# Optimization experiments

Measured on AMD Instinct MI355X. Metric: run time of the kernel, lower is better.

Reference implementation:

```python
import jax, jax.numpy as jnp
import numpy as np

M, D, NI, L, NPL, R, T = 2, 128, 131072, 4, 2048, 8, 32
N = NI + L * NPL  # total DAG nodes


def setup_inputs() -> dict:
    key = jax.random.key(0)
    ks = jax.random.split(key, 18)
    thax = jax.random.randint(ks[0], (NI,), 0, T)
    sine = jax.random.uniform(ks[1], (NI,), jnp.float32)
    # parents of layer-l deriv nodes index any node built earlier (topological)
    raw = jax.random.randint(ks[2], (L, NPL, 2), 0, 2**30)
    bounds = jnp.array([NI + l * NPL for l in range(L)])[:, None, None]
    par = raw % bounds
    ridx = jax.random.randint(ks[3], (L, NPL), 0, R)
    pos = jax.random.uniform(ks[4], (N,), jnp.float32) + 0.01
    neg = jax.random.uniform(ks[5], (N,), jnp.float32) + 0.01
    s = 0.05
    return {
        'thax': thax, 'sine': sine, 'par': par, 'ridx': ridx,
        'pos': pos, 'neg': neg,
        'init_table': jax.random.normal(ks[6], (M, T, D)) * s,
        's_vec': jax.random.normal(ks[7], (M, D)) * s,
        'W1': jax.random.normal(ks[8], (M, R, 2 * D, D)) * s,
        'b1': jax.random.normal(ks[9], (M, R, D)) * s,
        'W2': jax.random.normal(ks[10], (M, R, D, D)) * s,
        'b2': jax.random.normal(ks[11], (M, R, D)) * s,
        'tweaks': jax.random.normal(ks[12], (M, 1, 2)) * s,
        'We1': jax.random.normal(ks[13], (M, D, D)) * s,
        'be1': jax.random.normal(ks[14], (M, D)) * s,
        'we2': jax.random.normal(ks[15], (M, D)) * s,
        'be2': jax.random.normal(ks[16], (M,)) * s,
    }


def reference(thax, sine, par, ridx, pos, neg, init_table, s_vec,
              W1, b1, W2, b2, tweaks, We1, be1, we2, be2):
    # init nodes: thax embedding + sine embellishment (per model)
    emb0 = init_table[:, thax, :] + sine[None, :, None] * s_vec[:, None, :]  # [M,NI,D]
    store = jnp.zeros((M, N, D), emb0.dtype).at[:, :NI].set(emb0)
    # topological layers of deriv nodes: gather parents, rule-indexed 2-layer MLP
    for l in range(L):
        p, r = par[l], ridx[l]
        cat = store[:, p].reshape(M, NPL, 2 * D)               # gather parents
        h = jax.nn.relu(jnp.einsum('mnc,mncd->mnd', cat, W1[:, r]) + b1[:, r])
        out = (jnp.einsum('mnd,mnde->mne', h, W2[:, r]) + b2[:, r]
               + tweaks[:, 0, 1][:, None, None])
        store = store.at[:, NI + l * NPL: NI + (l + 1) * NPL].set(out)
    # eval_net: per-node scalar logit (+ per-problem tweak)
    he = jax.nn.relu(jnp.einsum('mnd,mde->mne', store, We1) + be1[:, None, :])
    logit = jnp.einsum('mnd,md->mn', he, we2) + be2[:, None] + tweaks[:, 0, 0][:, None]
    tot_pos, tot_neg = pos.sum(), neg.sum()
    pw = tot_neg / tot_pos  # POS_WEIGHT_EXTRA = 1.0
    gold = pos / (pos + neg)
    w = pos + neg
    # BCEWithLogitsLoss(pos_weight=pw) per node, weighted by (pos+neg)
    bce = -(pw * gold[None] * jax.nn.log_sigmoid(logit)
            + (1.0 - gold[None]) * jax.nn.log_sigmoid(-logit))
    loss = (w[None] * bce).sum(axis=1)                          # [M]
    posOK = jnp.where(logit >= 0, pos[None], 0.0).sum(axis=1)
    negOK = jnp.where(logit < 0, neg[None], 0.0).sum(axis=1)
    return (loss, posOK, negOK, tot_pos, tot_neg)
```

## Files before the change

### kernel.cpp

```cpp
#include <hip/hip_runtime.h>
#include <hip/hip_bf16.h>

#define M_ 2
#define D_ 128
#define NI_ 131072
#define L_ 4
#define NPL_ 2048
#define R_ 8
#define T_ 32
#define N_ (NI_ + L_ * NPL_)
#define ND_ (L_ * NPL_)
#define PART3_ 1344

typedef __bf16 bf16x8 __attribute__((ext_vector_type(8)));
typedef float f32x4 __attribute__((ext_vector_type(4)));

#define OFF_W1T    0u
#define OFF_W2T    1048576u
#define OFF_WE1T   1572864u
#define OFF_TAB    1638400u
#define OFF_SVEC   1654784u
#define OFF_SORTED 1655296u
#define OFF_STARTS 1688064u
#define OFF_CNTF   1688192u
#define OFF_CNTA   1688320u
#define OFF_EA2    1688448u
#define OFF_EWB    1721216u
#define OFF_PA     1723264u
#define OFF_PB     1734016u
#define OFF_PPOK   1744768u
#define OFF_PNOK   1755520u
#define OFF_PTP    1766272u
#define OFF_PTN    1771648u
#define OFF_G      1777024u
#define OFF_STORE  2317696u
#define OFF_FSG    6512000u
#define OFF_CFG    6512032u
#define OFF_FLIST  6512064u

__device__ __forceinline__ unsigned short f2bu(float f) {
  unsigned int u = __float_as_uint(f);
  u += 0x7fffu + ((u >> 16) & 1u);
  return (unsigned short)(u >> 16);
}
__device__ __forceinline__ bf16x8 ldb8(const unsigned short* p) {
  return *reinterpret_cast<const bf16x8*>(p);
}

__device__ __forceinline__ bf16x8 node_chunk(int m, int row, int d0,
    const unsigned short* tab, const unsigned short* svec,
    const unsigned short* sd, const int* thax, const float* sine) {
  if (row < NI_) {
    bf16x8 tv = ldb8(&tab[(m * T_ + thax[row]) * D_ + d0]);
    bf16x8 sv = ldb8(&svec[m * D_ + d0]);
    float sn = sine[row];
    bf16x8 r;
#pragma unroll
    for (int j = 0; j < 8; ++j)
      r[j] = (__bf16)((float)tv[j] + sn * (float)sv[j]);
    return r;
  }
  return ldb8(&sd[(size_t)(m * ND_ + (row - NI_)) * D_ + d0]);
}

__global__ __launch_bounds__(256) void megaprep_kernel(
    const float* W1, const float* W2, const float* We1,
    const float* init_table, const float* s_vec,
    const float* b1, const float* be1, const float* we2,
    const int* ridx, const int* par,
    unsigned short* W1T, unsigned short* W2T, unsigned short* We1T,
    unsigned short* tab, unsigned short* svec,
    float* G, float* EA2, float* EWB,
    int* sorted, int* starts, int* cntF, int* cntA,
    int* fsg, int* cfg, int* fastlist, unsigned int* pzero) {
  __shared__ float smem[1056];
  __shared__ int icnt[16], ioff[16];
  int job = blockIdx.x;
  int tid = threadIdx.x;

  if (job < 800) {
    int z, rblk, cblk;
    if (job < 512)      { z = job >> 5;            rblk = (job & 31) >> 2; cblk = job & 3; }
    else if (job < 768) { int q = job - 512; z = 16 + (q >> 4); rblk = (q & 15) >> 2; cblk = q & 3; }
    else                { int q = job - 768; z = 32 + (q >> 4); rblk = (q & 15) >> 2; cblk = q & 3; }
    const float* src; unsigned short* dst; int R;
    if (z < 16)      { src = W1  + (size_t)z * 32768;        dst = W1T  + (size_t)z * 32768;        R = 256; }
    else if (z < 32) { src = W2  + (size_t)(z - 16) * 16384; dst = W2T  + (size_t)(z - 16) * 16384; R = 128; }
    else             { src = We1 + (size_t)(z - 32) * 16384; dst = We1T + (size_t)(z - 32) * 16384; R = 128; }
    int r0 = rblk * 32, c0 = cblk * 32;
    float (*tile)[33] = (float(*)[33])smem;
    int tx = tid & 31, ty = tid >> 5;
#pragma unroll
    for (int k = 0; k < 4; ++k)
      tile[ty + 8 * k][tx] = src[(size_t)(r0 + ty + 8 * k) * D_ + c0 + tx];
    __syncthreads();
#pragma unroll
    for (int k = 0; k < 4; ++k)
      dst[(size_t)(c0 + ty + 8 * k) * R + r0 + tx] = f2bu(tile[tx][ty + 8 * k]);
  } else if (job == 800) {
    for (int i = tid; i < 8448; i += 256) {
      if (i < 8192) tab[i] = f2bu(init_table[i]);
      else svec[i - 8192] = f2bu(s_vec[i - 8192]);
    }
  } else if (job < 1329) {
    int q = job - 801;
    int t = q / 16, mr = q & 15;
    int m = mr >> 3;
    int slot = tid >> 7, e = tid & 127;
    const float* vec = (t < 32) ? &init_table[(size_t)(m * T_ + t) * D_]
                                : &s_vec[(size_t)m * D_];
    if (tid < 128) smem[tid] = vec[tid];
    __syncthreads();
    const float* w = &W1[((size_t)mr * 256 + slot * 128) * D_];
    float acc = 0.f;
#pragma unroll 8
    for (int c = 0; c < 128; ++c) acc = fmaf(smem[c], w[c * D_ + e], acc);
    if (slot == 0 && t < 32) acc += b1[mr * D_ + e];
    G[((size_t)(mr * 2 + slot) * 33 + t) * D_ + e] = acc;
  } else if (job < 1363) {
    int q = job - 1329;
    int m = q / 17, t = (q % 17) * 2 + (tid >> 7);
    int e = tid & 127;
    if (t <= 32) {
      const float* vec = (t < 32) ? &init_table[(size_t)(m * T_ + t) * D_]
                                  : &s_vec[(size_t)m * D_];
      const float* w = &We1[(size_t)m * D_ * D_];
      float acc = 0.f;
#pragma unroll 8
      for (int d = 0; d < 128; ++d) acc = fmaf(vec[d], w[d * D_ + e], acc);
      if (t < 32) {
        EA2[m * 4096 + ((e >> 1) * 32 + t) * 2 + (e & 1)] = acc + be1[m * D_ + e];
      } else {
        EWB[(m * D_ + e) * 2 + 0] = acc;
        EWB[(m * D_ + e) * 2 + 1] = we2[m * D_ + e];
      }
    }
  } else if (job < 1367) {
    int l = job - 1363;
    if (tid < 16) icnt[tid] = 0;
    __syncthreads();
    for (int n = tid; n < NPL_; n += 256) {
      int r = ridx[l * NPL_ + n];
      int p0 = par[(l * NPL_ + n) * 2 + 0], p1 = par[(l * NPL_ + n) * 2 + 1];
      int slow = (p0 >= NI_ || p1 >= NI_) ? 1 : 0;
      atomicAdd(&icnt[r * 2 + slow], 1);
    }
    __syncthreads();
    if (tid == 0) {
      int run = 0;
      for (int b = 0; b < 16; ++b) { ioff[b] = run; run += icnt[b]; }
      for (int r = 0; r < R_; ++r) {
        starts[l * R_ + r] = ioff[2 * r];
        cntF[l * R_ + r] = icnt[2 * r];
        cntA[l * R_ + r] = icnt[2 * r] + icnt[2 * r + 1];
      }
    }
    __syncthreads();
    for (int n = tid; n < NPL_; n += 256) {
      int r = ridx[l * NPL_ + n];
      int p0 = par[(l * NPL_ + n) * 2 + 0], p1 = par[(l * NPL_ + n) * 2 + 1];
      int slow = (p0 >= NI_ || p1 >= NI_) ? 1 : 0;
      int p = atomicAdd(&ioff[r * 2 + slow], 1);
      sorted[l * NPL_ + p] = n;
    }
  } else if (job == 1367) {
    if (tid < 8) icnt[tid] = 0;
    __syncthreads();
    for (int g = tid; g < ND_; g += 256) {
      int p0 = par[2 * g], p1 = par[2 * g + 1];
      if (p0 < NI_ && p1 < NI_) atomicAdd(&icnt[ridx[g]], 1);
    }
    __syncthreads();
    if (tid == 0) {
      int run = 0;
      for (int r = 0; r < R_; ++r) {
        ioff[r] = run; fsg[r] = run; cfg[r] = icnt[r]; run += icnt[r];
      }
    }
    __syncthreads();
    for (int g = tid; g < ND_; g += 256) {
      int p0 = par[2 * g], p1 = par[2 * g + 1];
      if (p0 < NI_ && p1 < NI_) {
        int p = atomicAdd(&ioff[ridx[g]], 1);
        fastlist[p] = g;
      }
    }
  } else {
    for (int i = tid; i < 13440; i += 256) pzero[i] = 0u;
  }
}

__global__ __launch_bounds__(256) void main_kernel(
    const int* thax, const float* sine, const int* par,
    const float* pos, const float* neg,
    const float* b2, const float* tweaks,
    const float* G, const unsigned short* W2T, const unsigned short* We1T,
    const float* EA2, const float* EWB,
    const float* be1, const float* we2, const float* be2,
    const int* fsg, const int* cfg, const int* fastlist,
    unsigned short* sd,
    float* pA, float* pB, float* pPok, float* pNok, float* pTp, float* pTn) {
  __shared__ float sbuf[4448];
  int bid = blockIdx.x;
  int tid = threadIdx.x;
  int w = tid >> 6, lane = tid & 63;

  if (bid < 1280) {
    int m = bid / 640, q = bid % 640;
    int r = q / 80, tile = q % 80;
    int cnt = cfg[r];
    int base = tile * 16;
    if (base >= cnt) return;
    unsigned short* h_lds = (unsigned short*)sbuf;
    int*   t0a  = (int*)(sbuf + 1024);
    int*   t1a  = t0a + 16;
    float* s0a  = (float*)(t1a + 16);
    float* s1a  = s0a + 16;
    int*   gida = (int*)(s1a + 16);
    float* red2 = sbuf + 1104;
    if (tid < 16) {
      int loc = base + tid; if (loc >= cnt) loc = cnt - 1;
      int gid = fastlist[fsg[r] + loc];
      int p0 = par[2 * gid], p1 = par[2 * gid + 1];
      t0a[tid] = thax[p0]; s0a[tid] = sine[p0];
      t1a[tid] = thax[p1]; s1a[tid] = sine[p1];
      gida[tid] = gid;
    }
    __syncthreads();
    const float* Gm = &G[(size_t)(m * R_ + r) * 8448];
    {
      int row = tid >> 4, seg = tid & 15, d0 = seg * 8;
      int t0 = t0a[row], t1 = t1a[row];
      float s0 = s0a[row], s1 = s1a[row];
      const float* pa = &Gm[t0 * 128 + d0];
      const float* pb = &Gm[(33 + t1) * 128 + d0];
      const float* pu = &Gm[4096 + d0];
      const float* pv = &Gm[8320 + d0];
      bf16x8 hv;
#pragma unroll
      for (int half = 0; half < 2; ++half) {
        float4 a = *(const float4*)(pa + half * 4);
        float4 b = *(const float4*)(pb + half * 4);
        float4 u = *(const float4*)(pu + half * 4);
        float4 v = *(const float4*)(pv + half * 4);
        hv[half * 4 + 0] = (__bf16)fmaxf(a.x + b.x + s0 * u.x + s1 * v.x, 0.f);
        hv[half * 4 + 1] = (__bf16)fmaxf(a.y + b.y + s0 * u.y + s1 * v.y, 0.f);
        hv[half * 4 + 2] = (__bf16)fmaxf(a.z + b.z + s0 * u.z + s1 * v.z, 0.f);
        hv[half * 4 + 3] = (__bf16)fmaxf(a.w + b.w + s0 * u.w + s1 * v.w, 0.f);
      }
      *(bf16x8*)&h_lds[row * 128 + (d0 ^ ((row & 7) << 3))] = hv;
    }
    __syncthreads();
    int l15 = lane & 15, l4 = lane >> 4;
    const unsigned short* w2b = &W2T[(size_t)(m * R_ + r) * D_ * D_];
    f32x4 acc[2];
    acc[0] = (f32x4){0.f, 0.f, 0.f, 0.f};
    acc[1] = (f32x4){0.f, 0.f, 0.f, 0.f};
#pragma unroll
    for (int kc = 0; kc < 4; ++kc) {
      int d0 = kc * 32 + l4 * 8;
      bf16x8 a2 = ldb8(&h_lds[l15 * 128 + (d0 ^ ((l15 & 7) << 3))]);
#pragma unroll
      for (int f = 0; f < 2; ++f) {
        int fg = w * 2 + f;
        bf16x8 b = ldb8(&w2b[(fg * 16 + l15) * D_ + d0]);
        acc[f] = __builtin_amdgcn_mfma_f32_16x16x32_bf16(a2, b, acc[f], 0, 0, 0);
      }
    }
    float tw1 = tweaks[m * 2 + 1];
    const float* b2v = &b2[(m * R_ + r) * D_];
    __syncthreads();
#pragma unroll
    for (int i = 0; i < 4; ++i) {
      int row = l4 * 4 + i;
      int g = base + row;
#pragma unroll
      for (int f = 0; f < 2; ++f) {
        int e = (w * 2 + f) * 16 + l15;
        unsigned short val = f2bu(acc[f][i] + b2v[e] + tw1);
        h_lds[row * 128 + (e ^ ((row & 7) << 3))] = val;
        if (g < cnt) sd[(size_t)(m * ND_ + gida[row]) * D_ + e] = val;
      }
    }
    __syncthreads();
    f32x4 ae[2];
    ae[0] = (f32x4){0.f, 0.f, 0.f, 0.f};
    ae[1] = (f32x4){0.f, 0.f, 0.f, 0.f};
    const unsigned short* we1b = &We1T[(size_t)m * D_ * D_];
#pragma unroll
    for (int kc = 0; kc < 4; ++kc) {
      int d0 = kc * 32 + l4 * 8;
      bf16x8 a2 = ldb8(&h_lds[l15 * 128 + (d0 ^ ((l15 & 7) << 3))]);
#pragma unroll
      for (int f = 0; f < 2; ++f) {
        int fg = w * 2 + f;
        bf16x8 b = ldb8(&we1b[(fg * 16 + l15) * D_ + d0]);
        ae[f] = __builtin_amdgcn_mfma_f32_16x16x32_bf16(a2, b, ae[f], 0, 0, 0);
      }
    }
    float part[4] = {0.f, 0.f, 0.f, 0.f};
#pragma unroll
    for (int f = 0; f < 2; ++f) {
      int e = (w * 2 + f) * 16 + l15;
      float bb = be1[m * D_ + e];
      float wv = we2[m * D_ + e];
#pragma unroll
      for (int i = 0; i < 4; ++i) {
        float he = ae[f][i] + bb;
        he = he > 0.f ? he : 0.f;
        part[i] += he * wv;
      }
    }
#pragma unroll
    for (int mask = 1; mask < 16; mask <<= 1) {
#pragma unroll
      for (int i = 0; i < 4; ++i) part[i] += __shfl_xor(part[i], mask, 64);
    }
    if (l15 == 0) {
#pragma unroll
      for (int i = 0; i < 4; ++i) red2[w * 16 + l4 * 4 + i] = part[i];
    }
    __syncthreads();
    if (tid < 16) {
      int g = base + tid;
      float v6[6] = {0.f, 0.f, 0.f, 0.f, 0.f, 0.f};
      if (g < cnt) {
        float logit = red2[tid] + red2[16 + tid] + red2[32 + tid] + red2[48 + tid]
                    + be2[m] + tweaks[m * 2 + 0];
        int grow = NI_ + gida[tid];
        float p_ = pos[grow], n_ = neg[grow];
        float lse = log1pf(__expf(-fabsf(logit)));
        v6[0] = p_ * (fmaxf(-logit, 0.f) + lse);
        v6[1] = n_ * (fmaxf(logit, 0.f) + lse);
        v6[2] = logit >= 0.f ? p_ : 0.f;
        v6[3] = logit < 0.f ? n_ : 0.f;
        v6[4] = p_; v6[5] = n_;
      }
#pragma unroll
      for (int mask = 1; mask < 16; mask <<= 1) {
#pragma unroll
        for (int qq = 0; qq < 6; ++qq) v6[qq] += __shfl_xor(v6[qq], mask, 64);
      }
      if (tid == 0) {
        int slot = 512 + r * 80 + tile;
        pA[m * PART3_ + slot] = v6[0];
        pB[m * PART3_ + slot] = v6[1];
        pPok[m * PART3_ + slot] = v6[2];
        pNok[m * PART3_ + slot] = v6[3];
        if (m == 0) { pTp[slot] = v6[4]; pTn[slot] = v6[5]; }
      }
    }
  } else {
    int q = bid - 1280;
    int m = q >> 9, xb = q & 511;
    float* lea = sbuf;
    float* lwb = sbuf + 4096;
    float* red = sbuf + 4352;
    for (int i = tid; i < 4096; i += 256) lea[i] = EA2[m * 4096 + i];
    if (tid < 256) lwb[tid] = EWB[m * 256 + tid];
    __syncthreads();
    int row = xb * 256 + tid;
    int t = thax[row];
    float s = sine[row];
    float acc = 0.f;
#pragma unroll 8
    for (int p = 0; p < 64; ++p) {
      float2 ea = *(const float2*)&lea[(p * 32 + t) * 2];
      float4 wb = *(const float4*)&lwb[p * 4];
      float x0 = fmaf(s, wb.x, ea.x); x0 = fmaxf(x0, 0.f);
      acc = fmaf(x0, wb.y, acc);
      float x1 = fmaf(s, wb.z, ea.y); x1 = fmaxf(x1, 0.f);
      acc = fmaf(x1, wb.w, acc);
    }
    float logit = acc + be2[m] + tweaks[m * 2 + 0];
    float p_ = pos[row], n_ = neg[row];
    float lse = log1pf(__expf(-fabsf(logit)));
    float v[6];
    v[0] = p_ * (fmaxf(-logit, 0.f) + lse);
    v[1] = n_ * (fmaxf(logit, 0.f) + lse);
    v[2] = logit >= 0.f ? p_ : 0.f;
    v[3] = logit < 0.f ? n_ : 0.f;
    v[4] = p_; v[5] = n_;
#pragma unroll
    for (int mask = 1; mask < 64; mask <<= 1) {
#pragma unroll
      for (int k = 0; k < 6; ++k) v[k] += __shfl_xor(v[k], mask, 64);
    }
    if (lane == 0) {
#pragma unroll
      for (int k = 0; k < 6; ++k) red[k * 16 + w] = v[k];
    }
    __syncthreads();
    if (tid == 0) {
      float t6[6];
#pragma unroll
      for (int k = 0; k < 6; ++k)
        t6[k] = red[k * 16 + 0] + red[k * 16 + 1] + red[k * 16 + 2] + red[k * 16 + 3];
      pA[m * PART3_ + xb] = t6[0];
      pB[m * PART3_ + xb] = t6[1];
      pPok[m * PART3_ + xb] = t6[2];
      pNok[m * PART3_ + xb] = t6[3];
      if (m == 0) { pTp[xb] = t6[4]; pTn[xb] = t6[5]; }
    }
  }
}

__global__ __launch_bounds__(128) void slow_eval_kernel(int l,
    const int* thax, const float* sine, const int* par,
    const float* b1, const float* b2, const float* tweaks,
    const float* pos, const float* neg,
    const float* be1, const float* we2, const float* be2,
    const unsigned short* tab, const unsigned short* svec,
    const unsigned short* W1T, const unsigned short* W2T,
    const unsigned short* We1T,
    const int* sorted, const int* starts, const int* cntF, const int* cntA,
    unsigned short* sd,
    float* pA, float* pB, float* pPok, float* pNok, float* pTp, float* pTn) {
  int tile = blockIdx.x, r = blockIdx.y, m = blockIdx.z;
  int cF = cntF[l * R_ + r];
  int cS = cntA[l * R_ + r] - cF;
  int base = tile * 16;
  if (base >= cS) return;
  int start = starts[l * R_ + r] + cF;
  int tid = threadIdx.x;
  int w = tid >> 6, lane = tid & 63;
  int l15 = lane & 15, l4 = lane >> 4;
  __shared__ unsigned short h_lds[16 * 128];
  __shared__ float red2[32];

  int loc = base + l15; if (loc >= cS) loc = cS - 1;
  int node = sorted[l * NPL_ + start + loc];
  int p0 = par[(l * NPL_ + node) * 2 + 0];
  int p1 = par[(l * NPL_ + node) * 2 + 1];
  const unsigned short* w1b = &W1T[(size_t)(m * R_ + r) * D_ * 256];
  const unsigned short* w2b = &W2T[(size_t)(m * R_ + r) * D_ * D_];
  const unsigned short* we1b = &We1T[(size_t)m * D_ * D_];

  bf16x8 av[8];
#pragma unroll
  for (int kc = 0; kc < 8; ++kc) {
    int k = kc * 32 + l4 * 8;
    int p = (k < 128) ? p0 : p1;
    av[kc] = node_chunk(m, p, k & 127, tab, svec, sd, thax, sine);
  }
  f32x4 acch[4];
#pragma unroll
  for (int f = 0; f < 4; ++f) acch[f] = (f32x4){0.f, 0.f, 0.f, 0.f};
#pragma unroll
  for (int kc = 0; kc < 8; ++kc) {
    int k = kc * 32 + l4 * 8;
#pragma unroll
    for (int f = 0; f < 4; ++f) {
      int fg = w * 4 + f;
      bf16x8 b = ldb8(&w1b[(fg * 16 + l15) * 256 + k]);
      acch[f] = __builtin_amdgcn_mfma_f32_16x16x32_bf16(av[kc], b, acch[f], 0, 0, 0);
    }
  }
  const float* b1v = &b1[(m * R_ + r) * D_];
#pragma unroll
  for (int f = 0; f < 4; ++f) {
    int d = (w * 4 + f) * 16 + l15;
    float bb = b1v[d];
#pragma unroll
    for (int i = 0; i < 4; ++i) {
      int row = l4 * 4 + i;
      float h = acch[f][i] + bb;
      h = h > 0.f ? h : 0.f;
      h_lds[row * 128 + (d ^ ((row & 7) << 3))] = f2bu(h);
    }
  }
  __syncthreads();
  f32x4 acco[4];
#pragma unroll
  for (int f = 0; f < 4; ++f) acco[f] = (f32x4){0.f, 0.f, 0.f, 0.f};
#pragma unroll
  for (int kc = 0; kc < 4; ++kc) {
    int d0 = kc * 32 + l4 * 8;
    bf16x8 a2 = ldb8(&h_lds[l15 * 128 + (d0 ^ ((l15 & 7) << 3))]);
#pragma unroll
    for (int f = 0; f < 4; ++f) {
      int fg = w * 4 + f;
      bf16x8 b = ldb8(&w2b[(fg * 16 + l15) * D_ + d0]);
      acco[f] = __builtin_amdgcn_mfma_f32_16x16x32_bf16(a2, b, acco[f], 0, 0, 0);
    }
  }
  float tw1 = tweaks[m * 2 + 1];
  const float* b2v = &b2[(m * R_ + r) * D_];
  __syncthreads();
#pragma unroll
  for (int i = 0; i < 4; ++i) {
    int row = l4 * 4 + i;
    int g = base + row;
#pragma unroll
    for (int f = 0; f < 4; ++f) {
      int e = (w * 4 + f) * 16 + l15;
      unsigned short val = f2bu(acco[f][i] + b2v[e] + tw1);
      h_lds[row * 128 + (e ^ ((row & 7) << 3))] = val;
      if (g < cS) {
        int nd = sorted[l * NPL_ + start + g];
        sd[(size_t)(m * ND_ + l * NPL_ + nd) * D_ + e] = val;
      }
    }
  }
  __syncthreads();
  f32x4 ae[4];
#pragma unroll
  for (int f = 0; f < 4; ++f) ae[f] = (f32x4){0.f, 0.f, 0.f, 0.f};
#pragma unroll
  for (int kc = 0; kc < 4; ++kc) {
    int d0 = kc * 32 + l4 * 8;
    bf16x8 a2 = ldb8(&h_lds[l15 * 128 + (d0 ^ ((l15 & 7) << 3))]);
#pragma unroll
    for (int f = 0; f < 4; ++f) {
      int fg = w * 4 + f;
      bf16x8 b = ldb8(&we1b[(fg * 16 + l15) * D_ + d0]);
      ae[f] = __builtin_amdgcn_mfma_f32_16x16x32_bf16(a2, b, ae[f], 0, 0, 0);
    }
  }
  float part[4] = {0.f, 0.f, 0.f, 0.f};
#pragma unroll
  for (int f = 0; f < 4; ++f) {
    int e = (w * 4 + f) * 16 + l15;
    float bb = be1[m * D_ + e];
    float wv = we2[m * D_ + e];
#pragma unroll
    for (int i = 0; i < 4; ++i) {
      float he = ae[f][i] + bb;
      he = he > 0.f ? he : 0.f;
      part[i] += he * wv;
    }
  }
#pragma unroll
  for (int mask = 1; mask < 16; mask <<= 1) {
#pragma unroll
    for (int i = 0; i < 4; ++i) part[i] += __shfl_xor(part[i], mask, 64);
  }
  if (l15 == 0) {
#pragma unroll
    for (int i = 0; i < 4; ++i) red2[w * 16 + l4 * 4 + i] = part[i];
  }
  __syncthreads();
  if (tid < 16) {
    int g = base + tid;
    float v6[6] = {0.f, 0.f, 0.f, 0.f, 0.f, 0.f};
    if (g < cS) {
      float logit = red2[tid] + red2[16 + tid] + be2[m] + tweaks[m * 2 + 0];
      int nd = sorted[l * NPL_ + start + g];
      int grow = NI_ + l * NPL_ + nd;
      float p_ = pos[grow], n_ = neg[grow];
      float lse = log1pf(__expf(-fabsf(logit)));
      v6[0] = p_ * (fmaxf(-logit, 0.f) + lse);
      v6[1] = n_ * (fmaxf(logit, 0.f) + lse);
      v6[2] = logit >= 0.f ? p_ : 0.f;
      v6[3] = logit < 0.f ? n_ : 0.f;
      v6[4] = p_; v6[5] = n_;
    }
#pragma unroll
    for (int mask = 1; mask < 16; mask <<= 1) {
#pragma unroll
      for (int qq = 0; qq < 6; ++qq) v6[qq] += __shfl_xor(v6[qq], mask, 64);
    }
    if (tid == 0) {
      int slot = 1152 + (l - 1) * 64 + r * 8 + tile;
      pA[m * PART3_ + slot] = v6[0];
      pB[m * PART3_ + slot] = v6[1];
      pPok[m * PART3_ + slot] = v6[2];
      pNok[m * PART3_ + slot] = v6[3];
      if (m == 0) { pTp[slot] = v6[4]; pTn[slot] = v6[5]; }
    }
  }
}

__global__ __launch_bounds__(256) void finalize_kernel(
    const float* pA, const float* pB, const float* pPok, const float* pNok,
    const float* pTp, const float* pTn, float* out) {
  __shared__ float lred[10][4];
  const float* srcs[10] = {pA, pA + PART3_, pB, pB + PART3_,
                           pPok, pPok + PART3_, pNok, pNok + PART3_,
                           pTp, pTn};
  int tid = threadIdx.x;
  int w = tid >> 6, lane = tid & 63;
#pragma unroll
  for (int q = 0; q < 10; ++q) {
    float s = 0.f;
    for (int i = tid; i < PART3_; i += 256) s += srcs[q][i];
#pragma unroll
    for (int mask = 1; mask < 64; mask <<= 1) s += __shfl_xor(s, mask, 64);
    if (lane == 0) lred[q][w] = s;
  }
  __syncthreads();
  if (tid == 0) {
    float totals[10];
#pragma unroll
    for (int q = 0; q < 10; ++q)
      totals[q] = lred[q][0] + lred[q][1] + lred[q][2] + lred[q][3];
    float tp = totals[8], tn = totals[9];
    float pw = tn / tp;
    out[0] = pw * totals[0] + totals[2];
    out[1] = pw * totals[1] + totals[3];
    out[2] = totals[4]; out[3] = totals[5];
    out[4] = totals[6]; out[5] = totals[7];
    out[6] = tp; out[7] = tn;
  }
}

extern "C" void kernel_launch(void* const* d_in, const int* in_sizes, int n_in,
                              void* d_out, int out_size, void* d_ws, size_t ws_size,
                              hipStream_t stream) {
  const int*   thax = (const int*)d_in[0];
  const float* sine = (const float*)d_in[1];
  const int*   par  = (const int*)d_in[2];
  const int*   ridx = (const int*)d_in[3];
  const float* pos  = (const float*)d_in[4];
  const float* neg  = (const float*)d_in[5];
  const float* init_table = (const float*)d_in[6];
  const float* s_vec = (const float*)d_in[7];
  const float* W1 = (const float*)d_in[8];
  const float* b1 = (const float*)d_in[9];
  const float* W2 = (const float*)d_in[10];
  const float* b2 = (const float*)d_in[11];
  const float* tweaks = (const float*)d_in[12];
  const float* We1 = (const float*)d_in[13];
  const float* be1 = (const float*)d_in[14];
  const float* we2 = (const float*)d_in[15];
  const float* be2 = (const float*)d_in[16];

  char* ws = (char*)d_ws;
  unsigned short* W1T  = (unsigned short*)(ws + OFF_W1T);
  unsigned short* W2T  = (unsigned short*)(ws + OFF_W2T);
  unsigned short* We1T = (unsigned short*)(ws + OFF_WE1T);
  unsigned short* tab  = (unsigned short*)(ws + OFF_TAB);
  unsigned short* svec = (unsigned short*)(ws + OFF_SVEC);
  int* sorted = (int*)(ws + OFF_SORTED);
  int* starts = (int*)(ws + OFF_STARTS);
  int* cntF   = (int*)(ws + OFF_CNTF);
  int* cntA   = (int*)(ws + OFF_CNTA);
  float* EA2  = (float*)(ws + OFF_EA2);
  float* EWB  = (float*)(ws + OFF_EWB);
  float* pA   = (float*)(ws + OFF_PA);
  float* pB   = (float*)(ws + OFF_PB);
  float* pPok = (float*)(ws + OFF_PPOK);
  float* pNok = (float*)(ws + OFF_PNOK);
  float* pTp  = (float*)(ws + OFF_PTP);
  float* pTn  = (float*)(ws + OFF_PTN);
  float* G    = (float*)(ws + OFF_G);
  unsigned short* sd = (unsigned short*)(ws + OFF_STORE);
  int* fsg      = (int*)(ws + OFF_FSG);
  int* cfg      = (int*)(ws + OFF_CFG);
  int* fastlist = (int*)(ws + OFF_FLIST);

  megaprep_kernel<<<1369, 256, 0, stream>>>(
      W1, W2, We1, init_table, s_vec, b1, be1, we2, ridx, par,
      W1T, W2T, We1T, tab, svec, G, EA2, EWB, sorted, starts, cntF, cntA,
      fsg, cfg, fastlist, (unsigned int*)pA);
  main_kernel<<<2304, 256, 0, stream>>>(
      thax, sine, par, pos, neg, b2, tweaks, G, W2T, We1T, EA2, EWB,
      be1, we2, be2, fsg, cfg, fastlist, sd,
      pA, pB, pPok, pNok, pTp, pTn);
  for (int l = 1; l < L_; ++l) {
    slow_eval_kernel<<<dim3(8, R_, M_), 128, 0, stream>>>(
        l, thax, sine, par, b1, b2, tweaks, pos, neg, be1, we2, be2,
        tab, svec, W1T, W2T, We1T, sorted, starts, cntF, cntA, sd,
        pA, pB, pPok, pNok, pTp, pTn);
  }
  finalize_kernel<<<1, 256, 0, stream>>>(pA, pB, pPok, pNok, pTp, pTn,
                                         (float*)d_out);
}
```

Before: 100.7 us.

## Merge per-layer slow-eval launches and finalize into one persistent tail kernel

Replaces the three per-layer slow_eval launches and the separate finalize launch with a single tail kernel of two 512-thread blocks, one per model. Each block walks layers 1..3 sequentially, with wavefronts taking tiles round-robin and using block barriers between layers in place of kernel boundaries. Each wavefront now computes all 128 output columns itself, using wave-local LDS waits instead of block syncs. Deriv-node pos/neg totals move into two extra main_kernel blocks, which shrinks the partial arrays. The aim is to cut launch and dependency gaps, at the cost of running the serial tail on only two CUs with less parallelism per layer.

Result: slower. 364.6 us (+262.1%).

```diff
diff --git a/kernel.cpp b/kernel.cpp
--- a/kernel.cpp
+++ b/kernel.cpp
@@ -10,7 +10,7 @@
 #define T_ 32
 #define N_ (NI_ + L_ * NPL_)
 #define ND_ (L_ * NPL_)
-#define PART3_ 1344
+#define PART4_ 1184
 
 typedef __bf16 bf16x8 __attribute__((ext_vector_type(8)));
 typedef float f32x4 __attribute__((ext_vector_type(4)));
@@ -27,16 +27,16 @@
 #define OFF_EA2    1688448u
 #define OFF_EWB    1721216u
 #define OFF_PA     1723264u
-#define OFF_PB     1734016u
-#define OFF_PPOK   1744768u
-#define OFF_PNOK   1755520u
-#define OFF_PTP    1766272u
-#define OFF_PTN    1771648u
-#define OFF_G      1777024u
-#define OFF_STORE  2317696u
-#define OFF_FSG    6512000u
-#define OFF_CFG    6512032u
-#define OFF_FLIST  6512064u
+#define OFF_PB     1732736u
+#define OFF_PPOK   1742208u
+#define OFF_PNOK   1751680u
+#define OFF_PTP    1761152u
+#define OFF_PTN    1765888u
+#define OFF_G      1770624u
+#define OFF_STORE  2311296u
+#define OFF_FSG    6505600u
+#define OFF_CFG    6505632u
+#define OFF_FLIST  6505664u
 
 __device__ __forceinline__ unsigned short f2bu(float f) {
   unsigned int u = __float_as_uint(f);
@@ -186,7 +186,7 @@
       }
     }
   } else {
-    for (int i = tid; i < 13440; i += 256) pzero[i] = 0u;
+    for (int i = tid; i < 11840; i += 256) pzero[i] = 0u;
   }
 }
 
@@ -323,7 +323,7 @@
     __syncthreads();
     if (tid < 16) {
       int g = base + tid;
-      float v6[6] = {0.f, 0.f, 0.f, 0.f, 0.f, 0.f};
+      float v6[4] = {0.f, 0.f, 0.f, 0.f};
       if (g < cnt) {
         float logit = red2[tid] + red2[16 + tid] + red2[32 + tid] + red2[48 + tid]
                     + be2[m] + tweaks[m * 2 + 0];
@@ -334,23 +334,21 @@
         v6[1] = n_ * (fmaxf(logit, 0.f) + lse);
         v6[2] = logit >= 0.f ? p_ : 0.f;
         v6[3] = logit < 0.f ? n_ : 0.f;
-        v6[4] = p_; v6[5] = n_;
       }
 #pragma unroll
       for (int mask = 1; mask < 16; mask <<= 1) {
 #pragma unroll
-        for (int qq = 0; qq < 6; ++qq) v6[qq] += __shfl_xor(v6[qq], mask, 64);
+        for (int qq = 0; qq < 4; ++qq) v6[qq] += __shfl_xor(v6[qq], mask, 64);
       }
       if (tid == 0) {
         int slot = 512 + r * 80 + tile;
-        pA[m * PART3_ + slot] = v6[0];
-        pB[m * PART3_ + slot] = v6[1];
-        pPok[m * PART3_ + slot] = v6[2];
-        pNok[m * PART3_ + slot] = v6[3];
-        if (m == 0) { pTp[slot] = v6[4]; pTn[slot] = v6[5]; }
-      }
-    }
-  } else {
+        pA[m * PART4_ + slot] = v6[0];
+        pB[m * PART4_ + slot] = v6[1];
+        pPok[m * PART4_ + slot] = v6[2];
+        pNok[m * PART4_ + slot] = v6[3];
+      }
+    }
+  } else if (bid < 2304) {
     int q = bid - 1280;
     int m = q >> 9, xb = q & 511;
     float* lea = sbuf;
@@ -396,16 +394,30 @@
 #pragma unroll
       for (int k = 0; k < 6; ++k)
         t6[k] = red[k * 16 + 0] + red[k * 16 + 1] + red[k * 16 + 2] + red[k * 16 + 3];
-      pA[m * PART3_ + xb] = t6[0];
-      pB[m * PART3_ + xb] = t6[1];
-      pPok[m * PART3_ + xb] = t6[2];
-      pNok[m * PART3_ + xb] = t6[3];
+      pA[m * PART4_ + xb] = t6[0];
+      pB[m * PART4_ + xb] = t6[1];
+      pPok[m * PART4_ + xb] = t6[2];
+      pNok[m * PART4_ + xb] = t6[3];
       if (m == 0) { pTp[xb] = t6[4]; pTn[xb] = t6[5]; }
     }
+  } else {
+    int j = bid - 2304;
+    float* red = sbuf;
+    const float* src = j ? neg : pos;
+    float s = 0.f;
+    for (int i = NI_ + tid; i < N_; i += 256) s += src[i];
+#pragma unroll
+    for (int mask = 1; mask < 64; mask <<= 1) s += __shfl_xor(s, mask, 64);
+    if (lane == 0) red[w] = s;
+    __syncthreads();
+    if (tid == 0) {
+      float t = red[0] + red[1] + red[2] + red[3];
+      if (j == 0) pTp[1152] = t; else pTn[1152] = t;
+    }
   }
 }
 
-__global__ __launch_bounds__(128) void slow_eval_kernel(int l,
+__global__ __launch_bounds__(512) void tail_kernel(
     const int* thax, const float* sine, const int* par,
     const float* b1, const float* b2, const float* tweaks,
     const float* pos, const float* neg,
@@ -415,192 +427,206 @@
     const unsigned short* We1T,
     const int* sorted, const int* starts, const int* cntF, const int* cntA,
     unsigned short* sd,
-    float* pA, float* pB, float* pPok, float* pNok, float* pTp, float* pTn) {
-  int tile = blockIdx.x, r = blockIdx.y, m = blockIdx.z;
-  int cF = cntF[l * R_ + r];
-  int cS = cntA[l * R_ + r] - cF;
-  int base = tile * 16;
-  if (base >= cS) return;
-  int start = starts[l * R_ + r] + cF;
-  int tid = threadIdx.x;
-  int w = tid >> 6, lane = tid & 63;
-  int l15 = lane & 15, l4 = lane >> 4;
-  __shared__ unsigned short h_lds[16 * 128];
-  __shared__ float red2[32];
-
-  int loc = base + l15; if (loc >= cS) loc = cS - 1;
-  int node = sorted[l * NPL_ + start + loc];
-  int p0 = par[(l * NPL_ + node) * 2 + 0];
-  int p1 = par[(l * NPL_ + node) * 2 + 1];
-  const unsigned short* w1b = &W1T[(size_t)(m * R_ + r) * D_ * 256];
-  const unsigned short* w2b = &W2T[(size_t)(m * R_ + r) * D_ * D_];
-  const unsigned short* we1b = &We1T[(size_t)m * D_ * D_];
-
-  bf16x8 av[8];
-#pragma unroll
-  for (int kc = 0; kc < 8; ++kc) {
-    int k = kc * 32 + l4 * 8;
-    int p = (k < 128) ? p0 : p1;
-    av[kc] = node_chunk(m, p, k & 127, tab, svec, sd, thax, sine);
-  }
-  f32x4 acch[4];
-#pragma unroll
-  for (int f = 0; f < 4; ++f) acch[f] = (f32x4){0.f, 0.f, 0.f, 0.f};
-#pragma unroll
-  for (int kc = 0; kc < 8; ++kc) {
-    int k = kc * 32 + l4 * 8;
-#pragma unroll
-    for (int f = 0; f < 4; ++f) {
-      int fg = w * 4 + f;
-      bf16x8 b = ldb8(&w1b[(fg * 16 + l15) * 256 + k]);
-      acch[f] = __builtin_amdgcn_mfma_f32_16x16x32_bf16(av[kc], b, acch[f], 0, 0, 0);
-    }
-  }
-  const float* b1v = &b1[(m * R_ + r) * D_];
-#pragma unroll
-  for (int f = 0; f < 4; ++f) {
-    int d = (w * 4 + f) * 16 + l15;
-    float bb = b1v[d];
-#pragma unroll
-    for (int i = 0; i < 4; ++i) {
-      int row = l4 * 4 + i;
-      float h = acch[f][i] + bb;
-      h = h > 0.f ? h : 0.f;
-      h_lds[row * 128 + (d ^ ((row & 7) << 3))] = f2bu(h);
-    }
-  }
-  __syncthreads();
-  f32x4 acco[4];
-#pragma unroll
-  for (int f = 0; f < 4; ++f) acco[f] = (f32x4){0.f, 0.f, 0.f, 0.f};
-#pragma unroll
-  for (int kc = 0; kc < 4; ++kc) {
-    int d0 = kc * 32 + l4 * 8;
-    bf16x8 a2 = ldb8(&h_lds[l15 * 128 + (d0 ^ ((l15 & 7) << 3))]);
-#pragma unroll
-    for (int f = 0; f < 4; ++f) {
-      int fg = w * 4 + f;
-      bf16x8 b = ldb8(&w2b[(fg * 16 + l15) * D_ + d0]);
-      acco[f] = __builtin_amdgcn_mfma_f32_16x16x32_bf16(a2, b, acco[f], 0, 0, 0);
-    }
-  }
-  float tw1 = tweaks[m * 2 + 1];
-  const float* b2v = &b2[(m * R_ + r) * D_];
-  __syncthreads();
-#pragma unroll
-  for (int i = 0; i < 4; ++i) {
-    int row = l4 * 4 + i;
-    int g = base + row;
-#pragma unroll
-    for (int f = 0; f < 4; ++f) {
-      int e = (w * 4 + f) * 16 + l15;
-      unsigned short val = f2bu(acco[f][i] + b2v[e] + tw1);
-      h_lds[row * 128 + (e ^ ((row & 7) << 3))] = val;
-      if (g < cS) {
-        int nd = sorted[l * NPL_ + start + g];
-        sd[(size_t)(m * ND_ + l * NPL_ + nd) * D_ + e] = val;
-      }
-    }
-  }
-  __syncthreads();
-  f32x4 ae[4];
-#pragma unroll
-  for (int f = 0; f < 4; ++f) ae[f] = (f32x4){0.f, 0.f, 0.f, 0.f};
-#pragma unroll
-  for (int kc = 0; kc < 4; ++kc) {
-    int d0 = kc * 32 + l4 * 8;
-    bf16x8 a2 = ldb8(&h_lds[l15 * 128 + (d0 ^ ((l15 & 7) << 3))]);
-#pragma unroll
-    for (int f = 0; f < 4; ++f) {
-      int fg = w * 4 + f;
-      bf16x8 b = ldb8(&we1b[(fg * 16 + l15) * D_ + d0]);
-      ae[f] = __builtin_amdgcn_mfma_f32_16x16x32_bf16(a2, b, ae[f], 0, 0, 0);
-    }
-  }
-  float part[4] = {0.f, 0.f, 0.f, 0.f};
-#pragma unroll
-  for (int f = 0; f < 4; ++f) {
-    int e = (w * 4 + f) * 16 + l15;
-    float bb = be1[m * D_ + e];
-    float wv = we2[m * D_ + e];
-#pragma unroll
-    for (int i = 0; i < 4; ++i) {
-      float he = ae[f][i] + bb;
-      he = he > 0.f ? he : 0.f;
-      part[i] += he * wv;
-    }
-  }
-#pragma unroll
-  for (int mask = 1; mask < 16; mask <<= 1) {
-#pragma unroll
-    for (int i = 0; i < 4; ++i) part[i] += __shfl_xor(part[i], mask, 64);
-  }
-  if (l15 == 0) {
-#pragma unroll
-    for (int i = 0; i < 4; ++i) red2[w * 16 + l4 * 4 + i] = part[i];
-  }
-  __syncthreads();
-  if (tid < 16) {
-    int g = base + tid;
-    float v6[6] = {0.f, 0.f, 0.f, 0.f, 0.f, 0.f};
-    if (g < cS) {
-      float logit = red2[tid] + red2[16 + tid] + be2[m] + tweaks[m * 2 + 0];
-      int nd = sorted[l * NPL_ + start + g];
-      int grow = NI_ + l * NPL_ + nd;
-      float p_ = pos[grow], n_ = neg[grow];
-      float lse = log1pf(__expf(-fabsf(logit)));
-      v6[0] = p_ * (fmaxf(-logit, 0.f) + lse);
-      v6[1] = n_ * (fmaxf(logit, 0.f) + lse);
-      v6[2] = logit >= 0.f ? p_ : 0.f;
-      v6[3] = logit < 0.f ? n_ : 0.f;
-      v6[4] = p_; v6[5] = n_;
-    }
-#pragma unroll
-    for (int mask = 1; mask < 16; mask <<= 1) {
-#pragma unroll
-      for (int qq = 0; qq < 6; ++qq) v6[qq] += __shfl_xor(v6[qq], mask, 64);
-    }
-    if (tid == 0) {
-      int slot = 1152 + (l - 1) * 64 + r * 8 + tile;
-      pA[m * PART3_ + slot] = v6[0];
-      pB[m * PART3_ + slot] = v6[1];
-      pPok[m * PART3_ + slot] = v6[2];
-      pNok[m * PART3_ + slot] = v6[3];
-      if (m == 0) { pTp[slot] = v6[4]; pTn[slot] = v6[5]; }
-    }
-  }
-}
-
-__global__ __launch_bounds__(256) void finalize_kernel(
     const float* pA, const float* pB, const float* pPok, const float* pNok,
     const float* pTp, const float* pTn, float* out) {
-  __shared__ float lred[10][4];
-  const float* srcs[10] = {pA, pA + PART3_, pB, pB + PART3_,
-                           pPok, pPok + PART3_, pNok, pNok + PART3_,
-                           pTp, pTn};
+  __shared__ unsigned short h_all[8][2048];
+  __shared__ float wred[8][6];
+  __shared__ float fin[8][6];
+  int m = blockIdx.x;
   int tid = threadIdx.x;
-  int w = tid >> 6, lane = tid & 63;
-#pragma unroll
-  for (int q = 0; q < 10; ++q) {
+  int unit = tid >> 6, lane = tid & 63;
+  int l15 = lane & 15, l4 = lane >> 4;
+  unsigned short* h_lds = h_all[unit];
+  float v6[6] = {0.f, 0.f, 0.f, 0.f, 0.f, 0.f};
+  float tw1 = tweaks[m * 2 + 1];
+  float tw0 = tweaks[m * 2 + 0];
+  float bev = be2[m];
+  const unsigned short* we1b = &We1T[(size_t)m * D_ * D_];
+
+  for (int l = 1; l < L_; ++l) {
+    int wcount = 0;
+    for (int r = 0; r < R_; ++r) {
+      int cF = cntF[l * R_ + r];
+      int cS = cntA[l * R_ + r] - cF;
+      int start = starts[l * R_ + r] + cF;
+      int nt = (cS + 15) >> 4;
+      const unsigned short* w1b = &W1T[(size_t)(m * R_ + r) * D_ * 256];
+      const unsigned short* w2b = &W2T[(size_t)(m * R_ + r) * D_ * D_];
+      const float* b1v = &b1[(m * R_ + r) * D_];
+      const float* b2v = &b2[(m * R_ + r) * D_];
+      for (int t = 0; t < nt; ++t, ++wcount) {
+        if ((wcount & 7) != unit) continue;
+        int base = t * 16;
+        int loc = base + l15; if (loc >= cS) loc = cS - 1;
+        int node = sorted[l * NPL_ + start + loc];
+        int p0 = par[(l * NPL_ + node) * 2 + 0];
+        int p1 = par[(l * NPL_ + node) * 2 + 1];
+        bf16x8 av[8];
+#pragma unroll
+        for (int kc = 0; kc < 8; ++kc) {
+          int k = kc * 32 + l4 * 8;
+          int p = (k < 128) ? p0 : p1;
+          av[kc] = node_chunk(m, p, k & 127, tab, svec, sd, thax, sine);
+        }
+        f32x4 acch[8];
+#pragma unroll
+        for (int f = 0; f < 8; ++f) acch[f] = (f32x4){0.f, 0.f, 0.f, 0.f};
+#pragma unroll
+        for (int kc = 0; kc < 8; ++kc) {
+          int k = kc * 32 + l4 * 8;
+#pragma unroll
+          for (int f = 0; f < 8; ++f) {
+            bf16x8 b = ldb8(&w1b[(f * 16 + l15) * 256 + k]);
+            acch[f] = __builtin_amdgcn_mfma_f32_16x16x32_bf16(av[kc], b, acch[f], 0, 0, 0);
+          }
+        }
+#pragma unroll
+        for (int f = 0; f < 8; ++f) {
+          int d = f * 16 + l15;
+          float bb = b1v[d];
+#pragma unroll
+          for (int i = 0; i < 4; ++i) {
+            int row = l4 * 4 + i;
+            float h = acch[f][i] + bb;
+            h = h > 0.f ? h : 0.f;
+            h_lds[row * 128 + (d ^ ((row & 7) << 3))] = f2bu(h);
+          }
+        }
+        asm volatile("s_waitcnt lgkmcnt(0)" ::: "memory");
+        __builtin_amdgcn_sched_barrier(0);
+        f32x4 acco[8];
+#pragma unroll
+        for (int f = 0; f < 8; ++f) acco[f] = (f32x4){0.f, 0.f, 0.f, 0.f};
+#pragma unroll
+        for (int kc = 0; kc < 4; ++kc) {
+          int d0 = kc * 32 + l4 * 8;
+          bf16x8 a2 = ldb8(&h_lds[l15 * 128 + (d0 ^ ((l15 & 7) << 3))]);
+#pragma unroll
+          for (int f = 0; f < 8; ++f) {
+            bf16x8 b = ldb8(&w2b[(f * 16 + l15) * D_ + d0]);
+            acco[f] = __builtin_amdgcn_mfma_f32_16x16x32_bf16(a2, b, acco[f], 0, 0, 0);
+          }
+        }
+        asm volatile("s_waitcnt lgkmcnt(0)" ::: "memory");
+        __builtin_amdgcn_sched_barrier(0);
+#pragma unroll
+        for (int i = 0; i < 4; ++i) {
+          int row = l4 * 4 + i;
+          int g = base + row;
+#pragma unroll
+          for (int f = 0; f < 8; ++f) {
+            int e = f * 16 + l15;
+            unsigned short val = f2bu(acco[f][i] + b2v[e] + tw1);
+            h_lds[row * 128 + (e ^ ((row & 7) << 3))] = val;
+            if (g < cS) {
+              int nd = sorted[l * NPL_ + start + g];
+              sd[(size_t)(m * ND_ + l * NPL_ + nd) * D_ + e] = val;
+            }
+          }
+        }
+        asm volatile("s_waitcnt lgkmcnt(0)" ::: "memory");
+        __builtin_amdgcn_sched_barrier(0);
+        f32x4 ae[8];
+#pragma unroll
+        for (int f = 0; f < 8; ++f) ae[f] = (f32x4){0.f, 0.f, 0.f, 0.f};
+#pragma unroll
+        for (int kc = 0; kc < 4; ++kc) {
+          int d0 = kc * 32 + l4 * 8;
+          bf16x8 a2 = ldb8(&h_lds[l15 * 128 + (d0 ^ ((l15 & 7) << 3))]);
+#pragma unroll
+          for (int f = 0; f < 8; ++f) {
+            bf16x8 b = ldb8(&we1b[(f * 16 + l15) * D_ + d0]);
+            ae[f] = __builtin_amdgcn_mfma_f32_16x16x32_bf16(a2, b, ae[f], 0, 0, 0);
+          }
+        }
+        float part[4] = {0.f, 0.f, 0.f, 0.f};
+#pragma unroll
+        for (int f = 0; f < 8; ++f) {
+          int e = f * 16 + l15;
+          float bb = be1[m * D_ + e];
+          float wv = we2[m * D_ + e];
+#pragma unroll
+          for (int i = 0; i < 4; ++i) {
+            float he = ae[f][i] + bb;
+            he = he > 0.f ? he : 0.f;
+            part[i] += he * wv;
+          }
+        }
+#pragma unroll
+        for (int mask = 1; mask < 16; mask <<= 1) {
+#pragma unroll
+          for (int i = 0; i < 4; ++i) part[i] += __shfl_xor(part[i], mask, 64);
+        }
+        if (l15 == 0) {
+#pragma unroll
+          for (int i = 0; i < 4; ++i) {
+            int g = base + l4 * 4 + i;
+            if (g < cS) {
+              int nd = sorted[l * NPL_ + start + g];
+              int grow = NI_ + l * NPL_ + nd;
+              float logit = part[i] + bev + tw0;
+              float p_ = pos[grow], n_ = neg[grow];
+              float lse = log1pf(__expf(-fabsf(logit)));
+              v6[0] += p_ * (fmaxf(-logit, 0.f) + lse);
+              v6[1] += n_ * (fmaxf(logit, 0.f) + lse);
+              if (logit >= 0.f) v6[2] += p_; else v6[3] += n_;
+            }
+          }
+        }
+      }
+    }
+    __syncthreads();
+  }
+#pragma unroll
+  for (int mask = 1; mask < 64; mask <<= 1) {
+#pragma unroll
+    for (int q = 0; q < 4; ++q) v6[q] += __shfl_xor(v6[q], mask, 64);
+  }
+  if (lane == 0) {
+#pragma unroll
+    for (int q = 0; q < 4; ++q) wred[unit][q] = v6[q];
+  }
+  float s6[6] = {0.f, 0.f, 0.f, 0.f, 0.f, 0.f};
+  const float* bases[6] = {pA + m * PART4_, pB + m * PART4_,
+                           pPok + m * PART4_, pNok + m * PART4_, pTp, pTn};
+#pragma unroll
+  for (int q = 0; q < 6; ++q) {
     float s = 0.f;
-    for (int i = tid; i < PART3_; i += 256) s += srcs[q][i];
-#pragma unroll
-    for (int mask = 1; mask < 64; mask <<= 1) s += __shfl_xor(s, mask, 64);
-    if (lane == 0) lred[q][w] = s;
+    for (int i = tid; i < PART4_; i += 512) s += bases[q][i];
+    s6[q] = s;
+  }
+#pragma unroll
+  for (int mask = 1; mask < 64; mask <<= 1) {
+#pragma unroll
+    for (int q = 0; q < 6; ++q) s6[q] += __shfl_xor(s6[q], mask, 64);
+  }
+  if (lane == 0) {
+#pragma unroll
+    for (int q = 0; q < 6; ++q) fin[unit][q] = s6[q];
   }
   __syncthreads();
   if (tid == 0) {
-    float totals[10];
-#pragma unroll
-    for (int q = 0; q < 10; ++q)
-      totals[q] = lred[q][0] + lred[q][1] + lred[q][2] + lred[q][3];
-    float tp = totals[8], tn = totals[9];
+    float tot[6], slow[4];
+#pragma unroll
+    for (int q = 0; q < 6; ++q) {
+      float s = 0.f;
+      for (int u = 0; u < 8; ++u) s += fin[u][q];
+      tot[q] = s;
+    }
+#pragma unroll
+    for (int q = 0; q < 4; ++q) {
+      float s = 0.f;
+      for (int u = 0; u < 8; ++u) s += wred[u][q];
+      slow[q] = s;
+    }
+    float SA = tot[0] + slow[0], SB = tot[1] + slow[1];
+    float SPok = tot[2] + slow[2], SNok = tot[3] + slow[3];
+    float tp = tot[4], tn = tot[5];
     float pw = tn / tp;
-    out[0] = pw * totals[0] + totals[2];
-    out[1] = pw * totals[1] + totals[3];
-    out[2] = totals[4]; out[3] = totals[5];
-    out[4] = totals[6]; out[5] = totals[7];
-    out[6] = tp; out[7] = tn;
+    out[0 + m] = pw * SA + SB;
+    out[2 + m] = SPok;
+    out[4 + m] = SNok;
+    if (m == 0) { out[6] = tp; out[7] = tn; }
   }
 }
 
@@ -653,16 +679,12 @@
       W1, W2, We1, init_table, s_vec, b1, be1, we2, ridx, par,
       W1T, W2T, We1T, tab, svec, G, EA2, EWB, sorted, starts, cntF, cntA,
       fsg, cfg, fastlist, (unsigned int*)pA);
-  main_kernel<<<2304, 256, 0, stream>>>(
+  main_kernel<<<2306, 256, 0, stream>>>(
       thax, sine, par, pos, neg, b2, tweaks, G, W2T, We1T, EA2, EWB,
       be1, we2, be2, fsg, cfg, fastlist, sd,
       pA, pB, pPok, pNok, pTp, pTn);
-  for (int l = 1; l < L_; ++l) {
-    slow_eval_kernel<<<dim3(8, R_, M_), 128, 0, stream>>>(
-        l, thax, sine, par, b1, b2, tweaks, pos, neg, be1, we2, be2,
-        tab, svec, W1T, W2T, We1T, sorted, starts, cntF, cntA, sd,
-        pA, pB, pPok, pNok, pTp, pTn);
-  }
-  finalize_kernel<<<1, 256, 0, stream>>>(pA, pB, pPok, pNok, pTp, pTn,
-                                         (float*)d_out);
+  tail_kernel<<<2, 512, 0, stream>>>(
+      thax, sine, par, b1, b2, tweaks, pos, neg, be1, we2, be2,
+      tab, svec, W1T, W2T, We1T, sorted, starts, cntF, cntA, sd,
+      pA, pB, pPok, pNok, pTp, pTn, (float*)d_out);
 }
```
